# Performance work log

Measured on AMD Instinct MI355X. Metric: run time of the kernel, lower is better.

Reference implementation:

```python
import jax, jax.numpy as jnp
import numpy as np

T_LEN, E_LEN, BATCH, DIM = 32, 256, 16, 512  # topic_len, exp_len, batch, input=hidden size
HID = 512


def setup_inputs() -> dict:
    key = jax.random.key(0)
    k1, k2, k3, k4, k5, k6 = jax.random.split(key, 6)
    topic = jax.random.normal(k1, (T_LEN, BATCH, DIM), dtype=jnp.float32)
    exp_output = jax.random.normal(k2, (E_LEN, BATCH, DIM), dtype=jnp.float32)
    seq_mask = jax.random.bernoulli(k3, 0.1, (E_LEN, BATCH))  # True = masked exp position
    # nn.Linear(hidden+input, hidden): weight [HID, HID+DIM], bias [HID]
    lim1 = 1.0 / np.sqrt(HID + DIM)
    W_attn = jax.random.uniform(k4, (HID, HID + DIM), minval=-lim1, maxval=lim1, dtype=jnp.float32)
    b_attn = jax.random.uniform(k5, (HID,), minval=-lim1, maxval=lim1, dtype=jnp.float32)
    # nn.Linear(hidden, 1): weight [1, HID], bias [1]
    lim2 = 1.0 / np.sqrt(HID)
    kv, kb = jax.random.split(k6)
    v_score = jax.random.uniform(kv, (1, HID), minval=-lim2, maxval=lim2, dtype=jnp.float32)
    b_score = jax.random.uniform(kb, (1,), minval=-lim2, maxval=lim2, dtype=jnp.float32)
    return {"topic": topic, "exp_output": exp_output, "seq_mask": seq_mask,
            "W_attn": W_attn, "b_attn": b_attn, "v_score": v_score, "b_score": b_score}


def reference(topic, exp_output, seq_mask, W_attn, b_attn, v_score, b_score):
    # topic: [T, B, D]; exp_output: [E, B, D]; seq_mask: [E, B] bool
    D = topic.shape[2]
    # Split the concat-Linear: cat(topic, exp) @ W.T == topic @ W[:, :D].T + exp @ W[:, D:].T
    proj_t = jnp.einsum('tbd,hd->bth', topic, W_attn[:, :D])        # [B, T, H]
    proj_e = jnp.einsum('ebd,hd->beh', exp_output, W_attn[:, D:])   # [B, E, H]
    feat = jnp.tanh(proj_t[:, :, None, :] + proj_e[:, None, :, :] + b_attn)  # [B, T, E, H]
    energies = jnp.einsum('bteh,h->bte', feat, v_score[0]) + b_score[0]      # [B, T, E]
    # mask exp positions (broadcast over topic dim), as masked_fill(-1e12)
    energies = jnp.where(seq_mask.T[:, None, :], jnp.float32(-1e12), energies)
    attn_s1 = jax.nn.softmax(jnp.swapaxes(energies, 1, 2), axis=2)  # [B, E, T], softmax over topics
    attn_s2 = jax.nn.softmax(energies, axis=2)                      # [B, T, E], softmax over exp
    new_exp = jnp.einsum('bet,btd->bed', attn_s1, jnp.swapaxes(topic, 0, 1))       # [B, E, D]
    new_topic = jnp.einsum('bte,bed->btd', attn_s2, jnp.swapaxes(exp_output, 0, 1))  # [B, T, D]
    return new_topic, new_exp
```

## Files before the change

### kernel.cpp

```cpp
#include <hip/hip_runtime.h>
#include <hip/hip_bf16.h>
#include <cstddef>
#include <cstdint>

#define T_LEN 32
#define E_LEN 256
#define BATCH 16
#define DIM 512
#define HID 512
#define WROW 1024

#define TWO_LOG2E 2.8853900817779268f
#define LOG2E 1.4426950408889634f

typedef __attribute__((ext_vector_type(8))) short bf16x8;
typedef __attribute__((ext_vector_type(4))) float f32x4;

__device__ inline bf16x8 cvt8(float4 a, float4 b) {
    union { bf16x8 v; __hip_bfloat16 h[8]; } u;
    u.h[0] = __float2bfloat16(a.x); u.h[1] = __float2bfloat16(a.y);
    u.h[2] = __float2bfloat16(a.z); u.h[3] = __float2bfloat16(a.w);
    u.h[4] = __float2bfloat16(b.x); u.h[5] = __float2bfloat16(b.y);
    u.h[6] = __float2bfloat16(b.z); u.h[7] = __float2bfloat16(b.w);
    return u.v;
}

#define GPAD 8
#define GLDR (64 + GPAD)

__global__ __launch_bounds__(256) void gemm_fused_k(
    const float* __restrict__ topic, const float* __restrict__ expo,
    const float* __restrict__ W, const float* __restrict__ battn,
    float* __restrict__ EPT, __hip_bfloat16* __restrict__ EPE) {
    __shared__ __align__(16) __hip_bfloat16 As[2][64 * GLDR];
    __shared__ __align__(16) __hip_bfloat16 Bs[2][64 * GLDR];
    const int tid = threadIdx.x;
    const int by = blockIdx.x >> 3;
    const int n0 = (blockIdx.x & 7) * 64;
    const float* A; const float* Wp; int m0;
    const bool isT = (by < 8);
    if (isT) { A = topic; Wp = W;       m0 = by * 64; }
    else     { A = expo;  Wp = W + DIM; m0 = (by - 8) * 64; }
    const int w = tid >> 6;
    const int lane = tid & 63;
    const int l15 = lane & 15;
    const int g = lane >> 4;
    const int srow = tid >> 2;
    const int sc = tid & 3;

    f32x4 acc[4];
    const f32x4 z = {0.f, 0.f, 0.f, 0.f};
#pragma unroll
    for (int nt = 0; nt < 4; ++nt) acc[nt] = z;

    const float* ga = A + (size_t)(m0 + srow) * 512 + sc * 8;
    const float* gb = Wp + (size_t)(n0 + srow) * WROW + sc * 8;

    float4 a0 = *(const float4*)(ga);
    float4 a1 = *(const float4*)(ga + 4);
    float4 a2 = *(const float4*)(ga + 32);
    float4 a3 = *(const float4*)(ga + 36);
    float4 b0 = *(const float4*)(gb);
    float4 b1 = *(const float4*)(gb + 4);
    float4 b2 = *(const float4*)(gb + 32);
    float4 b3 = *(const float4*)(gb + 36);

    for (int kk = 0; kk < 8; ++kk) {
        const int cur = kk & 1;
        bf16x8 av0 = cvt8(a0, a1), av1 = cvt8(a2, a3);
        bf16x8 bv0 = cvt8(b0, b1), bv1 = cvt8(b2, b3);
        if (kk < 7) {
            ga += 64; gb += 64;
            a0 = *(const float4*)(ga);
            a1 = *(const float4*)(ga + 4);
            a2 = *(const float4*)(ga + 32);
            a3 = *(const float4*)(ga + 36);
            b0 = *(const float4*)(gb);
            b1 = *(const float4*)(gb + 4);
            b2 = *(const float4*)(gb + 32);
            b3 = *(const float4*)(gb + 36);
        }
        *(bf16x8*)&As[cur][srow * GLDR + sc * 8] = av0;
        *(bf16x8*)&As[cur][srow * GLDR + sc * 8 + 32] = av1;
        *(bf16x8*)&Bs[cur][srow * GLDR + sc * 8] = bv0;
        *(bf16x8*)&Bs[cur][srow * GLDR + sc * 8 + 32] = bv1;
        __syncthreads();
#pragma unroll
        for (int s = 0; s < 2; ++s) {
            bf16x8 af = *(const bf16x8*)&As[cur][(w * 16 + l15) * GLDR + (s * 4 + g) * 8];
#pragma unroll
            for (int nt = 0; nt < 4; ++nt) {
                bf16x8 bf = *(const bf16x8*)&Bs[cur][(nt * 16 + l15) * GLDR + (s * 4 + g) * 8];
                acc[nt] = __builtin_amdgcn_mfma_f32_16x16x32_bf16(af, bf, acc[nt], 0, 0, 0);
            }
        }
    }
    if (isT) {
#pragma unroll
        for (int nt = 0; nt < 4; ++nt) {
            int n = n0 + nt * 16 + l15;
            float bv = battn[n];
#pragma unroll
            for (int r = 0; r < 4; ++r) {
                int m = m0 + w * 16 + g * 4 + r;
                EPT[(size_t)m * 512 + n] =
                    __builtin_amdgcn_exp2f((acc[nt][r] + bv) * TWO_LOG2E);
            }
        }
    } else {
#pragma unroll
        for (int nt = 0; nt < 4; ++nt) {
            int n = n0 + nt * 16 + l15;
#pragma unroll
            for (int r = 0; r < 4; ++r) {
                int m = m0 + w * 16 + g * 4 + r;
                EPE[(size_t)m * 512 + n] = __float2bfloat16(
                    __builtin_amdgcn_exp2f(acc[nt][r] * TWO_LOG2E));
            }
        }
    }
}

__global__ __launch_bounds__(256) void energies_k(
    const float* __restrict__ EPT, const __hip_bfloat16* __restrict__ EPE,
    const float* __restrict__ v, const int* __restrict__ mask,
    float* __restrict__ P) {
    const int u = blockIdx.x;
    const int b = u & 15;
    const int tg = (u >> 4) & 3;
    const int ech = u >> 6;
    const int tid = threadIdx.x;
    const int lane = tid & 63;
    const int w = tid >> 6;
    const int h0 = lane * 8;
    const int e0 = ech * 16 + w * 4;

    int mk[4];
#pragma unroll
    for (int ei = 0; ei < 4; ++ei) mk[ei] = mask[(e0 + ei) * BATCH + b];

    float sv[8], sv2[4], spt[8][8];
    {
        float4 v0 = *(const float4*)(v + h0);
        float4 v1 = *(const float4*)(v + h0 + 4);
        sv[0] = -2.f * v0.x; sv[1] = -2.f * v0.y; sv[2] = -2.f * v0.z; sv[3] = -2.f * v0.w;
        sv[4] = -2.f * v1.x; sv[5] = -2.f * v1.y; sv[6] = -2.f * v1.z; sv[7] = -2.f * v1.w;
        sv2[0] = sv[0] + sv[1]; sv2[1] = sv[2] + sv[3];
        sv2[2] = sv[4] + sv[5]; sv2[3] = sv[6] + sv[7];
#pragma unroll
        for (int i = 0; i < 8; ++i) {
            const float* p = EPT + ((size_t)((tg * 8 + i) * BATCH + b)) * HID + h0;
            float4 p0 = *(const float4*)(p);
            float4 p1 = *(const float4*)(p + 4);
            spt[i][0] = p0.x; spt[i][1] = p0.y; spt[i][2] = p0.z; spt[i][3] = p0.w;
            spt[i][4] = p1.x; spt[i][5] = p1.y; spt[i][6] = p1.z; spt[i][7] = p1.w;
        }
    }
#pragma unroll
    for (int ei = 0; ei < 4; ++ei) {
        const int e = e0 + ei;
        if (mk[ei] != 0) {
            if (lane < 8)
                P[((size_t)b * T_LEN + tg * 8 + lane) * E_LEN + e] = 1e-30f;
            continue;
        }
        union { bf16x8 v8; __hip_bfloat16 h[8]; } pv;
        pv.v8 = *(const bf16x8*)(EPE + ((size_t)(e * BATCH + b)) * HID + h0);
        float pr[8];
#pragma unroll
        for (int j = 0; j < 8; ++j) pr[j] = __bfloat162float(pv.h[j]);
        float a[8] = {0.f, 0.f, 0.f, 0.f, 0.f, 0.f, 0.f, 0.f};
#pragma unroll
        for (int i = 0; i < 8; ++i) {
#pragma unroll
            for (int jq = 0; jq < 2; ++jq) {
                const int j0 = jq * 4;
                float a0 = spt[i][j0 + 0] * pr[j0 + 0];
                float a1 = spt[i][j0 + 1] * pr[j0 + 1];
                float a2 = spt[i][j0 + 2] * pr[j0 + 2];
                float a3 = spt[i][j0 + 3] * pr[j0 + 3];
                float u0 = a0 + 1.0f;
                float u2 = a2 + 1.0f;
                float d01 = fmaf(a1, u0, u0);
                float d23 = fmaf(a3, u2, u2);
                float n01 = fmaf(sv[j0 + 0], a1, fmaf(sv[j0 + 1], a0, sv2[jq * 2 + 0]));
                float n23 = fmaf(sv[j0 + 2], a3, fmaf(sv[j0 + 3], a2, sv2[jq * 2 + 1]));
                float nn = fmaf(n01, d23, n23 * d01);
                float dd = d01 * d23;
                a[i] = fmaf(nn, __builtin_amdgcn_rcpf(dd), a[i]);
            }
        }
#pragma unroll
        for (int i = 0; i < 8; ++i) {
            a[i] += __shfl_xor(a[i], 1);
            a[i] += __shfl_xor(a[i], 2);
            a[i] += __shfl_xor(a[i], 4);
            a[i] += __shfl_xor(a[i], 8);
        }
        const int sel = lane & 3;
        float uA = sel == 0 ? a[0] : sel == 1 ? a[1] : sel == 2 ? a[2] : a[3];
        float uB = sel == 0 ? a[4] : sel == 1 ? a[5] : sel == 2 ? a[6] : a[7];
        uA += __shfl_xor(uA, 16); uA += __shfl_xor(uA, 32);
        uB += __shfl_xor(uB, 16); uB += __shfl_xor(uB, 32);
        float uu = (lane & 4) ? uB : uA;
        if (lane < 8)
            P[((size_t)b * T_LEN + tg * 8 + lane) * E_LEN + e] =
                __builtin_amdgcn_exp2f(uu * LOG2E);
    }
}

__global__ __launch_bounds__(256) void epilogue_k(
    const float* __restrict__ P, const float* __restrict__ topic,
    const float* __restrict__ expo, float* __restrict__ out) {
    __shared__ __align__(16) float smem[5120];
    const int tid = threadIdx.x;
    const int lane = tid & 63;
    const int w = tid >> 6;
    if (blockIdx.x < 512) {
        const int b = blockIdx.x >> 5;
        const int ech = (blockIdx.x >> 1) & 15;
        const int hf = blockIdx.x & 1;
        const int e0 = ech * 16 + w * 4;
        float wv[4];
#pragma unroll
        for (int ei = 0; ei < 4; ++ei) {
            const int e = e0 + ei;
            float x = (lane < T_LEN) ? P[((size_t)b * T_LEN + lane) * E_LEN + e] : 0.f;
            float s = x;
#pragma unroll
            for (int off = 32; off; off >>= 1) s += __shfl_xor(s, off);
            wv[ei] = x * __builtin_amdgcn_rcpf(s);
        }
        const int d0 = hf * 256 + lane * 4;
        float4 acc[4];
#pragma unroll
        for (int ei = 0; ei < 4; ++ei) acc[ei] = {0.f, 0.f, 0.f, 0.f};
        for (int t = 0; t < T_LEN; ++t) {
            float4 r = *(const float4*)(topic + ((size_t)t * BATCH + b) * DIM + d0);
            float wt[4];
#pragma unroll
            for (int ei = 0; ei < 4; ++ei) wt[ei] = __shfl(wv[ei], t);
#pragma unroll
            for (int ei = 0; ei < 4; ++ei) {
                acc[ei].x = fmaf(wt[ei], r.x, acc[ei].x);
                acc[ei].y = fmaf(wt[ei], r.y, acc[ei].y);
                acc[ei].z = fmaf(wt[ei], r.z, acc[ei].z);
                acc[ei].w = fmaf(wt[ei], r.w, acc[ei].w);
            }
        }
#pragma unroll
        for (int ei = 0; ei < 4; ++ei) {
            float* o = out + (size_t)BATCH * T_LEN * DIM +
                       ((size_t)b * E_LEN + e0 + ei) * DIM + d0;
            *(float4*)o = acc[ei];
        }
    } else {
        const int q = blockIdx.x - 512;
        const int b = q >> 4;
        const int tq = (q >> 1) & 7;
        const int hf = q & 1;
        {
            const int bt = b * T_LEN + tq * 4 + w;
            float4 xv = *(const float4*)&P[(size_t)bt * E_LEN + lane * 4];
            float s = xv.x + xv.y + xv.z + xv.w;
#pragma unroll
            for (int off = 32; off; off >>= 1) s += __shfl_xor(s, off);
            float inv = __builtin_amdgcn_rcpf(s);
            float4 wvv = {xv.x * inv, xv.y * inv, xv.z * inv, xv.w * inv};
            *(float4*)&smem[w * 256 + lane * 4] = wvv;
        }
        __syncthreads();
        const int dl = lane * 4;
        const int dglob = hf * 256 + dl;
        float4 a0 = {0.f, 0.f, 0.f, 0.f};
        float4 a1 = {0.f, 0.f, 0.f, 0.f};
        float4 a2 = {0.f, 0.f, 0.f, 0.f};
        float4 a3 = {0.f, 0.f, 0.f, 0.f};
        const float* base = expo + (size_t)b * DIM + dglob;
        for (int ee = 0; ee < 64; ++ee) {
            const int e = w * 64 + ee;
            float4 rv = *(const float4*)(base + (size_t)e * BATCH * DIM);
            float w0 = smem[e];
            float w1 = smem[256 + e];
            float w2 = smem[512 + e];
            float w3 = smem[768 + e];
            a0.x = fmaf(w0, rv.x, a0.x); a0.y = fmaf(w0, rv.y, a0.y);
            a0.z = fmaf(w0, rv.z, a0.z); a0.w = fmaf(w0, rv.w, a0.w);
            a1.x = fmaf(w1, rv.x, a1.x); a1.y = fmaf(w1, rv.y, a1.y);
            a1.z = fmaf(w1, rv.z, a1.z); a1.w = fmaf(w1, rv.w, a1.w);
            a2.x = fmaf(w2, rv.x, a2.x); a2.y = fmaf(w2, rv.y, a2.y);
            a2.z = fmaf(w2, rv.z, a2.z); a2.w = fmaf(w2, rv.w, a2.w);
            a3.x = fmaf(w3, rv.x, a3.x); a3.y = fmaf(w3, rv.y, a3.y);
            a3.z = fmaf(w3, rv.z, a3.z); a3.w = fmaf(w3, rv.w, a3.w);
        }
        *(float4*)&smem[1024 + (w * 4 + 0) * 256 + dl] = a0;
        *(float4*)&smem[1024 + (w * 4 + 1) * 256 + dl] = a1;
        *(float4*)&smem[1024 + (w * 4 + 2) * 256 + dl] = a2;
        *(float4*)&smem[1024 + (w * 4 + 3) * 256 + dl] = a3;
        __syncthreads();
#pragma unroll
        for (int tt = 0; tt < 4; ++tt) {
            float sum = smem[1024 + (0 * 4 + tt) * 256 + tid] +
                        smem[1024 + (1 * 4 + tt) * 256 + tid] +
                        smem[1024 + (2 * 4 + tt) * 256 + tid] +
                        smem[1024 + (3 * 4 + tt) * 256 + tid];
            out[((size_t)b * T_LEN + tq * 4 + tt) * DIM + hf * 256 + tid] = sum;
        }
    }
}

extern "C" void kernel_launch(void* const* d_in, const int* in_sizes, int n_in,
                              void* d_out, int out_size, void* d_ws, size_t ws_size,
                              hipStream_t stream) {
    const float* topic = (const float*)d_in[0];
    const float* expo  = (const float*)d_in[1];
    const int*   mask  = (const int*)d_in[2];
    const float* W     = (const float*)d_in[3];
    const float* battn = (const float*)d_in[4];
    const float* vsc   = (const float*)d_in[5];
    float* out = (float*)d_out;

    float* EPT = (float*)d_ws;
    __hip_bfloat16* EPE = (__hip_bfloat16*)(EPT + 512 * 512);
    float* P = (float*)(EPE + (size_t)4096 * 512);

    gemm_fused_k<<<576, 256, 0, stream>>>(topic, expo, W, battn, EPT, EPE);
    energies_k<<<1024, 256, 0, stream>>>(EPT, EPE, vsc, mask, P);
    epilogue_k<<<768, 256, 0, stream>>>(P, topic, expo, out);
}
```

Before: 113.6 us.

## Write transposed probability copy and tighten reductions and weight staging in epilogue

The energies kernel now writes a second, transposed copy of the exponentiated scores so the exp-side epilogue reads 32 contiguous topic values per position instead of strided gathers. The 8-way butterfly reduction is rewritten as a recursive-halving pattern that uses fewer shuffles. In the epilogue, softmax weights are staged through shared memory and read as float4 instead of using per-iteration lane shuffles, and the topic-side weights are stored interleaved so one float4 LDS load replaces four scalar loads. This costs extra global writes of the transposed buffer and an additional block barrier.

```diff
diff --git a/kernel.cpp b/kernel.cpp
--- a/kernel.cpp
+++ b/kernel.cpp
@@ -124,7 +124,7 @@
 __global__ __launch_bounds__(256) void energies_k(
     const float* __restrict__ EPT, const __hip_bfloat16* __restrict__ EPE,
     const float* __restrict__ v, const int* __restrict__ mask,
-    float* __restrict__ P) {
+    float* __restrict__ P, float* __restrict__ PT) {
     const int u = blockIdx.x;
     const int b = u & 15;
     const int tg = (u >> 4) & 3;
@@ -134,6 +134,9 @@
     const int w = tid >> 6;
     const int h0 = lane * 8;
     const int e0 = ech * 16 + w * 4;
+    const bool o1 = (lane & 1) != 0;
+    const bool o2 = (lane & 2) != 0;
+    const bool o4 = (lane & 4) != 0;
 
     int mk[4];
 #pragma unroll
@@ -160,8 +163,10 @@
     for (int ei = 0; ei < 4; ++ei) {
         const int e = e0 + ei;
         if (mk[ei] != 0) {
-            if (lane < 8)
+            if (lane < 8) {
                 P[((size_t)b * T_LEN + tg * 8 + lane) * E_LEN + e] = 1e-30f;
+                PT[((size_t)b * E_LEN + e) * T_LEN + tg * 8 + lane] = 1e-30f;
+            }
             continue;
         }
         union { bf16x8 v8; __hip_bfloat16 h[8]; } pv;
@@ -190,27 +195,28 @@
                 a[i] = fmaf(nn, __builtin_amdgcn_rcpf(dd), a[i]);
             }
         }
-#pragma unroll
-        for (int i = 0; i < 8; ++i) {
-            a[i] += __shfl_xor(a[i], 1);
-            a[i] += __shfl_xor(a[i], 2);
-            a[i] += __shfl_xor(a[i], 4);
-            a[i] += __shfl_xor(a[i], 8);
-        }
-        const int sel = lane & 3;
-        float uA = sel == 0 ? a[0] : sel == 1 ? a[1] : sel == 2 ? a[2] : a[3];
-        float uB = sel == 0 ? a[4] : sel == 1 ? a[5] : sel == 2 ? a[6] : a[7];
-        uA += __shfl_xor(uA, 16); uA += __shfl_xor(uA, 32);
-        uB += __shfl_xor(uB, 16); uB += __shfl_xor(uB, 32);
-        float uu = (lane & 4) ? uB : uA;
-        if (lane < 8)
-            P[((size_t)b * T_LEN + tg * 8 + lane) * E_LEN + e] =
-                __builtin_amdgcn_exp2f(uu * LOG2E);
+        float s, b0, b1, b2, b3, d0, d1, f;
+        s = __shfl_xor(o1 ? a[0] : a[1], 1); b0 = (o1 ? a[1] : a[0]) + s;
+        s = __shfl_xor(o1 ? a[2] : a[3], 1); b1 = (o1 ? a[3] : a[2]) + s;
+        s = __shfl_xor(o1 ? a[4] : a[5], 1); b2 = (o1 ? a[5] : a[4]) + s;
+        s = __shfl_xor(o1 ? a[6] : a[7], 1); b3 = (o1 ? a[7] : a[6]) + s;
+        s = __shfl_xor(o2 ? b0 : b1, 2); d0 = (o2 ? b1 : b0) + s;
+        s = __shfl_xor(o2 ? b2 : b3, 2); d1 = (o2 ? b3 : b2) + s;
+        s = __shfl_xor(o4 ? d0 : d1, 4); f = (o4 ? d1 : d0) + s;
+        f += __shfl_xor(f, 8);
+        f += __shfl_xor(f, 16);
+        f += __shfl_xor(f, 32);
+        if (lane < 8) {
+            float pe = __builtin_amdgcn_exp2f(f * LOG2E);
+            P[((size_t)b * T_LEN + tg * 8 + lane) * E_LEN + e] = pe;
+            PT[((size_t)b * E_LEN + e) * T_LEN + tg * 8 + lane] = pe;
+        }
     }
 }
 
 __global__ __launch_bounds__(256) void epilogue_k(
-    const float* __restrict__ P, const float* __restrict__ topic,
+    const float* __restrict__ P, const float* __restrict__ PT,
+    const float* __restrict__ topic,
     const float* __restrict__ expo, float* __restrict__ out) {
     __shared__ __align__(16) float smem[5120];
     const int tid = threadIdx.x;
@@ -221,31 +227,42 @@
         const int ech = (blockIdx.x >> 1) & 15;
         const int hf = blockIdx.x & 1;
         const int e0 = ech * 16 + w * 4;
-        float wv[4];
 #pragma unroll
         for (int ei = 0; ei < 4; ++ei) {
             const int e = e0 + ei;
-            float x = (lane < T_LEN) ? P[((size_t)b * T_LEN + lane) * E_LEN + e] : 0.f;
+            float x = 0.f;
+            if (lane < T_LEN)
+                x = PT[((size_t)b * E_LEN + e) * T_LEN + lane];
             float s = x;
 #pragma unroll
             for (int off = 32; off; off >>= 1) s += __shfl_xor(s, off);
-            wv[ei] = x * __builtin_amdgcn_rcpf(s);
-        }
+            float wv = x * __builtin_amdgcn_rcpf(s);
+            if (lane < T_LEN) smem[(w * 4 + ei) * 32 + lane] = wv;
+        }
+        __syncthreads();
         const int d0 = hf * 256 + lane * 4;
         float4 acc[4];
 #pragma unroll
         for (int ei = 0; ei < 4; ++ei) acc[ei] = {0.f, 0.f, 0.f, 0.f};
-        for (int t = 0; t < T_LEN; ++t) {
-            float4 r = *(const float4*)(topic + ((size_t)t * BATCH + b) * DIM + d0);
-            float wt[4];
-#pragma unroll
-            for (int ei = 0; ei < 4; ++ei) wt[ei] = __shfl(wv[ei], t);
+#pragma unroll 2
+        for (int tq = 0; tq < 8; ++tq) {
+            float wqa[4][4];
 #pragma unroll
             for (int ei = 0; ei < 4; ++ei) {
-                acc[ei].x = fmaf(wt[ei], r.x, acc[ei].x);
-                acc[ei].y = fmaf(wt[ei], r.y, acc[ei].y);
-                acc[ei].z = fmaf(wt[ei], r.z, acc[ei].z);
-                acc[ei].w = fmaf(wt[ei], r.w, acc[ei].w);
+                float4 q = *(const float4*)&smem[(w * 4 + ei) * 32 + tq * 4];
+                wqa[ei][0] = q.x; wqa[ei][1] = q.y; wqa[ei][2] = q.z; wqa[ei][3] = q.w;
+            }
+#pragma unroll
+            for (int tt = 0; tt < 4; ++tt) {
+                const int t = tq * 4 + tt;
+                float4 r = *(const float4*)(topic + ((size_t)t * BATCH + b) * DIM + d0);
+#pragma unroll
+                for (int ei = 0; ei < 4; ++ei) {
+                    acc[ei].x = fmaf(wqa[ei][tt], r.x, acc[ei].x);
+                    acc[ei].y = fmaf(wqa[ei][tt], r.y, acc[ei].y);
+                    acc[ei].z = fmaf(wqa[ei][tt], r.z, acc[ei].z);
+                    acc[ei].w = fmaf(wqa[ei][tt], r.w, acc[ei].w);
+                }
             }
         }
 #pragma unroll
@@ -266,8 +283,10 @@
 #pragma unroll
             for (int off = 32; off; off >>= 1) s += __shfl_xor(s, off);
             float inv = __builtin_amdgcn_rcpf(s);
-            float4 wvv = {xv.x * inv, xv.y * inv, xv.z * inv, xv.w * inv};
-            *(float4*)&smem[w * 256 + lane * 4] = wvv;
+            smem[(lane * 4 + 0) * 4 + w] = xv.x * inv;
+            smem[(lane * 4 + 1) * 4 + w] = xv.y * inv;
+            smem[(lane * 4 + 2) * 4 + w] = xv.z * inv;
+            smem[(lane * 4 + 3) * 4 + w] = xv.w * inv;
         }
         __syncthreads();
         const int dl = lane * 4;
@@ -280,18 +299,15 @@
         for (int ee = 0; ee < 64; ++ee) {
             const int e = w * 64 + ee;
             float4 rv = *(const float4*)(base + (size_t)e * BATCH * DIM);
-            float w0 = smem[e];
-            float w1 = smem[256 + e];
-            float w2 = smem[512 + e];
-            float w3 = smem[768 + e];
-            a0.x = fmaf(w0, rv.x, a0.x); a0.y = fmaf(w0, rv.y, a0.y);
-            a0.z = fmaf(w0, rv.z, a0.z); a0.w = fmaf(w0, rv.w, a0.w);
-            a1.x = fmaf(w1, rv.x, a1.x); a1.y = fmaf(w1, rv.y, a1.y);
-            a1.z = fmaf(w1, rv.z, a1.z); a1.w = fmaf(w1, rv.w, a1.w);
-            a2.x = fmaf(w2, rv.x, a2.x); a2.y = fmaf(w2, rv.y, a2.y);
-            a2.z = fmaf(w2, rv.z, a2.z); a2.w = fmaf(w2, rv.w, a2.w);
-            a3.x = fmaf(w3, rv.x, a3.x); a3.y = fmaf(w3, rv.y, a3.y);
-            a3.z = fmaf(w3, rv.z, a3.z); a3.w = fmaf(w3, rv.w, a3.w);
+            float4 wq = *(const float4*)&smem[e * 4];
+            a0.x = fmaf(wq.x, rv.x, a0.x); a0.y = fmaf(wq.x, rv.y, a0.y);
+            a0.z = fmaf(wq.x, rv.z, a0.z); a0.w = fmaf(wq.x, rv.w, a0.w);
+            a1.x = fmaf(wq.y, rv.x, a1.x); a1.y = fmaf(wq.y, rv.y, a1.y);
+            a1.z = fmaf(wq.y, rv.z, a1.z); a1.w = fmaf(wq.y, rv.w, a1.w);
+            a2.x = fmaf(wq.z, rv.x, a2.x); a2.y = fmaf(wq.z, rv.y, a2.y);
+            a2.z = fmaf(wq.z, rv.z, a2.z); a2.w = fmaf(wq.z, rv.w, a2.w);
+            a3.x = fmaf(wq.w, rv.x, a3.x); a3.y = fmaf(wq.w, rv.y, a3.y);
+            a3.z = fmaf(wq.w, rv.z, a3.z); a3.w = fmaf(wq.w, rv.w, a3.w);
         }
         *(float4*)&smem[1024 + (w * 4 + 0) * 256 + dl] = a0;
         *(float4*)&smem[1024 + (w * 4 + 1) * 256 + dl] = a1;
@@ -322,9 +338,10 @@
 
     float* EPT = (float*)d_ws;
     __hip_bfloat16* EPE = (__hip_bfloat16*)(EPT + 512 * 512);
-    float* P = (float*)(EPE + (size_t)4096 * 512);
+    float* P  = (float*)(EPE + (size_t)4096 * 512);
+    float* PT = P + (size_t)BATCH * T_LEN * E_LEN;
 
     gemm_fused_k<<<576, 256, 0, stream>>>(topic, expo, W, battn, EPT, EPE);
-    energies_k<<<1024, 256, 0, stream>>>(EPT, EPE, vsc, mask, P);
-    epilogue_k<<<768, 256, 0, stream>>>(P, topic, expo, out);
-}
+    energies_k<<<1024, 256, 0, stream>>>(EPT, EPE, vsc, mask, P, PT);
+    epilogue_k<<<768, 256, 0, stream>>>(P, PT, topic, expo, out);
+}
```

After: 111.2 us. -2.2%, faster.
